# Optimization experiments

Hardware: AMD Instinct MI355X
Metric: run time of the kernel (lower is better)

The kernel has to match this reference:

```python
import jax, jax.numpy as jnp
import numpy as np

B, N, F, H = 64, 1024, 128, 256  # graphs, nodes per graph, nfeat, nhid


def setup_inputs() -> dict:
    key = jax.random.key(0)
    ks = jax.random.split(key, 8)
    s_in = 1.0 / np.sqrt(F)
    s_h = 1.0 / np.sqrt(H)
    return {
        "embs": jax.random.normal(ks[0], (B, N, F), jnp.float32),
        "adjmat": jax.random.uniform(ks[1], (B, N, N), jnp.float32) / N,  # row-scaled dense adjacency
        "W0": jax.random.normal(ks[2], (F, H), jnp.float32) * s_in,
        "b0": jnp.zeros((H,), jnp.float32),
        "W1": jax.random.normal(ks[3], (H, H), jnp.float32) * s_h,
        "b1": jnp.zeros((H,), jnp.float32),
        "W2": jax.random.normal(ks[4], (H, H), jnp.float32) * s_h,
        "b2": jnp.zeros((H,), jnp.float32),
        "Wl": jax.random.normal(ks[5], (H, F), jnp.float32) * s_h,
        "bl": jnp.zeros((F,), jnp.float32),
    }


def reference(embs, adjmat, W0, b0, W1, b1, W2, b2, Wl, bl):
    # Batched form of the per-graph loop: every adj is N x N, so the
    # x[:adj.shape[0]] slice is identity and all graphs fuse into one GEMM.
    hid = embs  # [B, N, F]
    for W, b in ((W0, b0), (W1, b1), (W2, b2)):
        # GraphConvolution: adj @ (x @ W) + b, then relu
        hid = jax.nn.relu(jnp.einsum('bnm,bmh->bnh', adjmat, hid @ W) + b)
    out = hid @ Wl + bl          # [B, N, F] linear_hid
    return out[:, 0, :]          # hid[0] per graph -> [B, F]
```

## Files before the change

kernel.cpp:

```cpp
#include <hip/hip_runtime.h>
#include <stdint.h>

typedef __bf16 bf16;
typedef __bf16 bf16x8 __attribute__((ext_vector_type(8)));
typedef float f32x4 __attribute__((ext_vector_type(4)));

enum { EPI_STORE = 0, EPI_BIAS_RELU = 1, EPI_VRED = 2 };

template<bool A_F32, bool B_F32, int EPI>
__global__ __launch_bounds__(256, 2)
void gemm_bt(const void* __restrict__ Ap, const void* __restrict__ Btp,
             const float* __restrict__ bias, bf16* __restrict__ C,
             float* __restrict__ vpart, const float* __restrict__ adjp,
             int K, int ldA, int ldBt, int ldC,
             long sA, long sBt, long sC)
{
  constexpr int BM = 128, BN = 256, BK = 32;
  __shared__ __align__(16) bf16 As[BM * BK];
  __shared__ __align__(16) bf16 Bs[BN * BK];
  __shared__ float a0s[BM];
  __shared__ float vsum[BN];

  const int tid  = threadIdx.x;
  const int lane = tid & 63;
  const int wid  = tid >> 6;
  const int wm   = wid >> 1;
  const int wn   = wid & 1;
  const int l15  = lane & 15;
  const int quad = lane >> 4;

  const int nb = blockIdx.x, mb = blockIdx.y, g = blockIdx.z;

  const long aoff = (long)g * sA + (long)mb * BM * ldA;
  const long boff = (long)g * sBt + (long)nb * BN * ldBt;

  if constexpr (EPI == EPI_VRED) {
    if (tid < BM) a0s[tid] = adjp[(long)g * sA + mb * BM + tid];
    vsum[tid] = 0.f;
  }

  f32x4 acc[4][8] = {};

  const int nsteps = K / BK;
  const int r  = tid >> 2;
  const int kc = (tid & 3) * 8;

  for (int ks = 0; ks < nsteps; ++ks) {
    const int k0 = ks * BK;
    __syncthreads();
    if constexpr (A_F32) {
      const float* Ag = (const float*)Ap + aoff + k0;
      #pragma unroll
      for (int p = 0; p < BM / 64; ++p) {
        const float4* s = (const float4*)(Ag + (long)(p * 64 + r) * ldA + kc);
        float4 v0 = s[0], v1 = s[1];
        bf16x8 w;
        w[0]=(bf16)v0.x; w[1]=(bf16)v0.y; w[2]=(bf16)v0.z; w[3]=(bf16)v0.w;
        w[4]=(bf16)v1.x; w[5]=(bf16)v1.y; w[6]=(bf16)v1.z; w[7]=(bf16)v1.w;
        *(bf16x8*)&As[p * 2048 + tid * 8] = w;
      }
    } else {
      const bf16* Ag = (const bf16*)Ap + aoff + k0;
      #pragma unroll
      for (int p = 0; p < BM / 64; ++p)
        *(bf16x8*)&As[p * 2048 + tid * 8] =
            *(const bf16x8*)(Ag + (long)(p * 64 + r) * ldA + kc);
    }
    if constexpr (B_F32) {
      const float* Bg = (const float*)Btp + boff + k0;
      #pragma unroll
      for (int p = 0; p < BN / 64; ++p) {
        const float4* s = (const float4*)(Bg + (long)(p * 64 + r) * ldBt + kc);
        float4 v0 = s[0], v1 = s[1];
        bf16x8 w;
        w[0]=(bf16)v0.x; w[1]=(bf16)v0.y; w[2]=(bf16)v0.z; w[3]=(bf16)v0.w;
        w[4]=(bf16)v1.x; w[5]=(bf16)v1.y; w[6]=(bf16)v1.z; w[7]=(bf16)v1.w;
        *(bf16x8*)&Bs[p * 2048 + tid * 8] = w;
      }
    } else {
      const bf16* Bg = (const bf16*)Btp + boff + k0;
      #pragma unroll
      for (int p = 0; p < BN / 64; ++p)
        *(bf16x8*)&Bs[p * 2048 + tid * 8] =
            *(const bf16x8*)(Bg + (long)(p * 64 + r) * ldBt + kc);
    }
    __syncthreads();

    bf16x8 af[4], bfr[8];
    #pragma unroll
    for (int i = 0; i < 4; ++i)
      af[i] = *(const bf16x8*)&As[(wm * 64 + i * 16 + l15) * BK + quad * 8];
    #pragma unroll
    for (int j = 0; j < 8; ++j)
      bfr[j] = *(const bf16x8*)&Bs[(wn * 128 + j * 16 + l15) * BK + quad * 8];
    #pragma unroll
    for (int i = 0; i < 4; ++i)
      #pragma unroll
      for (int j = 0; j < 8; ++j)
        acc[i][j] = __builtin_amdgcn_mfma_f32_16x16x32_bf16(af[i], bfr[j], acc[i][j], 0, 0, 0);
  }

  if constexpr (EPI == EPI_STORE || EPI == EPI_BIAS_RELU) {
    bf16* Cg = C + (long)g * sC;
    #pragma unroll
    for (int i = 0; i < 4; ++i) {
      const int row0 = mb * BM + wm * 64 + i * 16 + quad * 4;
      #pragma unroll
      for (int j = 0; j < 8; ++j) {
        const int col = nb * BN + wn * 128 + j * 16 + l15;
        float bv = 0.f;
        if constexpr (EPI == EPI_BIAS_RELU) bv = bias[col];
        #pragma unroll
        for (int rr = 0; rr < 4; ++rr) {
          float v = acc[i][j][rr];
          if constexpr (EPI == EPI_BIAS_RELU) v = fmaxf(v + bv, 0.f);
          Cg[(long)(row0 + rr) * ldC + col] = (bf16)v;
        }
      }
    }
  } else {
    __syncthreads();
    #pragma unroll
    for (int j = 0; j < 8; ++j) {
      const int col = wn * 128 + j * 16 + l15;
      const float bv = bias[col];
      float p = 0.f;
      #pragma unroll
      for (int i = 0; i < 4; ++i) {
        const int lr = wm * 64 + i * 16 + quad * 4;
        #pragma unroll
        for (int rr = 0; rr < 4; ++rr)
          p += fmaxf(acc[i][j][rr] + bv, 0.f) * a0s[lr + rr];
      }
      atomicAdd(&vsum[col], p);
    }
    __syncthreads();
    vpart[((long)g * 8 + mb) * 256 + tid] = vsum[tid];
  }
}

__global__ void prep_w(const float* __restrict__ W0, const float* __restrict__ W1,
                       bf16* __restrict__ W0t, bf16* __restrict__ W1t)
{
  const int idx = blockIdx.x * 256 + threadIdx.x;
  if (idx < 256 * 128) {
    const int h = idx >> 7, k = idx & 127;
    W0t[idx] = (bf16)W0[k * 256 + h];
  }
  const int h = idx >> 8, k = idx & 255;
  W1t[idx] = (bf16)W1[k * 256 + h];
}

__global__ void finish_k(const float* __restrict__ vpart, const float* __restrict__ W2,
                         const float* __restrict__ b2, const float* __restrict__ Wl,
                         const float* __restrict__ bl, float* __restrict__ out)
{
  const int b = blockIdx.x, t = threadIdx.x;
  __shared__ float v[256], h3[256];
  float s = 0.f;
  #pragma unroll
  for (int mb = 0; mb < 8; ++mb) s += vpart[((long)b * 8 + mb) * 256 + t];
  v[t] = s;
  __syncthreads();
  float z = b2[t];
  for (int k = 0; k < 256; ++k) z += v[k] * W2[k * 256 + t];
  h3[t] = fmaxf(z, 0.f);
  __syncthreads();
  if (t < 128) {
    float o = bl[t];
    for (int h = 0; h < 256; ++h) o += h3[h] * Wl[h * 128 + t];
    out[(long)b * 128 + t] = o;
  }
}

extern "C" void kernel_launch(void* const* d_in, const int* in_sizes, int n_in,
                              void* d_out, int out_size, void* d_ws, size_t ws_size,
                              hipStream_t stream) {
  const float* embs = (const float*)d_in[0];
  const float* adj  = (const float*)d_in[1];
  const float* W0   = (const float*)d_in[2];
  const float* b0   = (const float*)d_in[3];
  const float* W1   = (const float*)d_in[4];
  const float* b1   = (const float*)d_in[5];
  const float* W2   = (const float*)d_in[6];
  const float* b2   = (const float*)d_in[7];
  const float* Wl   = (const float*)d_in[8];
  const float* bl   = (const float*)d_in[9];
  float* out = (float*)d_out;

  char* ws = (char*)d_ws;
  bf16*  Zt    = (bf16*)(ws);
  bf16*  Hb    = (bf16*)(ws + 33554432);
  bf16*  W0t   = (bf16*)(ws + 67108864);
  bf16*  W1t   = (bf16*)(ws + 67174400);
  float* vpart = (float*)(ws + 67305472);

  prep_w<<<256, 256, 0, stream>>>(W0, W1, W0t, W1t);

  gemm_bt<false, true, EPI_STORE><<<dim3(4, 2, 64), 256, 0, stream>>>(
      W0t, embs, nullptr, Zt, nullptr, nullptr,
      128, 128, 128, 1024, 0L, 131072L, 262144L);

  gemm_bt<true, false, EPI_BIAS_RELU><<<dim3(1, 8, 64), 256, 0, stream>>>(
      adj, Zt, b0, Hb, nullptr, nullptr,
      1024, 1024, 1024, 256, 1048576L, 262144L, 262144L);

  gemm_bt<false, false, EPI_STORE><<<dim3(4, 2, 64), 256, 0, stream>>>(
      W1t, Hb, nullptr, Zt, nullptr, nullptr,
      256, 256, 256, 1024, 0L, 262144L, 262144L);

  gemm_bt<true, false, EPI_VRED><<<dim3(1, 8, 64), 256, 0, stream>>>(
      adj, Zt, b1, nullptr, vpart, adj,
      1024, 1024, 1024, 256, 1048576L, 262144L, 0L);

  finish_k<<<64, 256, 0, stream>>>(vpart, W2, b2, Wl, bl, out);
}
```

Baseline: 569.6 us.

## Pre-convert adjacency to bf16 and stream tiles via direct global-to-LDS loads

Adds a conversion kernel that turns adj and embs into bf16 buffers once, so both adjacency GEMMs read half the bytes instead of converting fp32 in registers twice. The GEMM loads now use global_load_lds so tiles go straight into shared memory without passing through registers. BM is halved to 64 with occupancy hint 3, doubling the grid and the partial-sum count in finish_k. The cost is an extra full pass over the 256MB fp32 adjacency plus a 128MB bf16 write, and an extra kernel launch.

```diff
diff --git a/kernel.cpp b/kernel.cpp
--- a/kernel.cpp
+++ b/kernel.cpp
@@ -7,15 +7,20 @@
 
 enum { EPI_STORE = 0, EPI_BIAS_RELU = 1, EPI_VRED = 2 };
 
-template<bool A_F32, bool B_F32, int EPI>
-__global__ __launch_bounds__(256, 2)
-void gemm_bt(const void* __restrict__ Ap, const void* __restrict__ Btp,
+__device__ __forceinline__ void load_lds16(const bf16* g, bf16* l) {
+  __builtin_amdgcn_global_load_lds((const __attribute__((address_space(1))) void*)g,
+                                   (__attribute__((address_space(3))) void*)l, 16, 0, 0);
+}
+
+template<int EPI>
+__global__ __launch_bounds__(256, 3)
+void gemm_bt(const bf16* __restrict__ Ap, const bf16* __restrict__ Btp,
              const float* __restrict__ bias, bf16* __restrict__ C,
-             float* __restrict__ vpart, const float* __restrict__ adjp,
+             float* __restrict__ vpart, const bf16* __restrict__ a0p,
              int K, int ldA, int ldBt, int ldC,
              long sA, long sBt, long sC)
 {
-  constexpr int BM = 128, BN = 256, BK = 32;
+  constexpr int BM = 64, BN = 256, BK = 32;
   __shared__ __align__(16) bf16 As[BM * BK];
   __shared__ __align__(16) bf16 Bs[BN * BK];
   __shared__ float a0s[BM];
@@ -24,77 +29,41 @@
   const int tid  = threadIdx.x;
   const int lane = tid & 63;
   const int wid  = tid >> 6;
-  const int wm   = wid >> 1;
-  const int wn   = wid & 1;
+  const int wm   = wid & 1;
+  const int wn   = wid >> 1;
   const int l15  = lane & 15;
   const int quad = lane >> 4;
 
   const int nb = blockIdx.x, mb = blockIdx.y, g = blockIdx.z;
 
-  const long aoff = (long)g * sA + (long)mb * BM * ldA;
-  const long boff = (long)g * sBt + (long)nb * BN * ldBt;
+  const bf16* Ag = Ap + (long)g * sA + (long)(mb * BM + (tid >> 2)) * ldA + (tid & 3) * 8;
+  const bf16* Bg = Btp + (long)g * sBt + (long)(nb * BN + (tid >> 2)) * ldBt + (tid & 3) * 8;
+  const long bstep = (long)64 * ldBt;
 
   if constexpr (EPI == EPI_VRED) {
-    if (tid < BM) a0s[tid] = adjp[(long)g * sA + mb * BM + tid];
+    if (tid < BM) a0s[tid] = (float)a0p[(long)g * sA + mb * BM + tid];
     vsum[tid] = 0.f;
   }
 
-  f32x4 acc[4][8] = {};
-
-  const int nsteps = K / BK;
-  const int r  = tid >> 2;
-  const int kc = (tid & 3) * 8;
-
-  for (int ks = 0; ks < nsteps; ++ks) {
-    const int k0 = ks * BK;
-    __syncthreads();
-    if constexpr (A_F32) {
-      const float* Ag = (const float*)Ap + aoff + k0;
-      #pragma unroll
-      for (int p = 0; p < BM / 64; ++p) {
-        const float4* s = (const float4*)(Ag + (long)(p * 64 + r) * ldA + kc);
-        float4 v0 = s[0], v1 = s[1];
-        bf16x8 w;
-        w[0]=(bf16)v0.x; w[1]=(bf16)v0.y; w[2]=(bf16)v0.z; w[3]=(bf16)v0.w;
-        w[4]=(bf16)v1.x; w[5]=(bf16)v1.y; w[6]=(bf16)v1.z; w[7]=(bf16)v1.w;
-        *(bf16x8*)&As[p * 2048 + tid * 8] = w;
-      }
-    } else {
-      const bf16* Ag = (const bf16*)Ap + aoff + k0;
-      #pragma unroll
-      for (int p = 0; p < BM / 64; ++p)
-        *(bf16x8*)&As[p * 2048 + tid * 8] =
-            *(const bf16x8*)(Ag + (long)(p * 64 + r) * ldA + kc);
-    }
-    if constexpr (B_F32) {
-      const float* Bg = (const float*)Btp + boff + k0;
-      #pragma unroll
-      for (int p = 0; p < BN / 64; ++p) {
-        const float4* s = (const float4*)(Bg + (long)(p * 64 + r) * ldBt + kc);
-        float4 v0 = s[0], v1 = s[1];
-        bf16x8 w;
-        w[0]=(bf16)v0.x; w[1]=(bf16)v0.y; w[2]=(bf16)v0.z; w[3]=(bf16)v0.w;
-        w[4]=(bf16)v1.x; w[5]=(bf16)v1.y; w[6]=(bf16)v1.z; w[7]=(bf16)v1.w;
-        *(bf16x8*)&Bs[p * 2048 + tid * 8] = w;
-      }
-    } else {
-      const bf16* Bg = (const bf16*)Btp + boff + k0;
-      #pragma unroll
-      for (int p = 0; p < BN / 64; ++p)
-        *(bf16x8*)&Bs[p * 2048 + tid * 8] =
-            *(const bf16x8*)(Bg + (long)(p * 64 + r) * ldBt + kc);
-    }
-    __syncthreads();
-
-    bf16x8 af[4], bfr[8];
-    #pragma unroll
-    for (int i = 0; i < 4; ++i)
-      af[i] = *(const bf16x8*)&As[(wm * 64 + i * 16 + l15) * BK + quad * 8];
+  f32x4 acc[2][8] = {};
+
+  for (int ks = 0; ks < K; ks += BK) {
+    __syncthreads();
+    load_lds16(Ag + ks, As + tid * 8);
+    #pragma unroll
+    for (int p = 0; p < 4; ++p)
+      load_lds16(Bg + p * bstep + ks, Bs + p * 2048 + tid * 8);
+    __syncthreads();
+
+    bf16x8 af[2], bfr[8];
+    #pragma unroll
+    for (int i = 0; i < 2; ++i)
+      af[i] = *(const bf16x8*)&As[(wm * 32 + i * 16 + l15) * BK + quad * 8];
     #pragma unroll
     for (int j = 0; j < 8; ++j)
       bfr[j] = *(const bf16x8*)&Bs[(wn * 128 + j * 16 + l15) * BK + quad * 8];
     #pragma unroll
-    for (int i = 0; i < 4; ++i)
+    for (int i = 0; i < 2; ++i)
       #pragma unroll
       for (int j = 0; j < 8; ++j)
         acc[i][j] = __builtin_amdgcn_mfma_f32_16x16x32_bf16(af[i], bfr[j], acc[i][j], 0, 0, 0);
@@ -103,8 +72,8 @@
   if constexpr (EPI == EPI_STORE || EPI == EPI_BIAS_RELU) {
     bf16* Cg = C + (long)g * sC;
     #pragma unroll
-    for (int i = 0; i < 4; ++i) {
-      const int row0 = mb * BM + wm * 64 + i * 16 + quad * 4;
+    for (int i = 0; i < 2; ++i) {
+      const int row0 = mb * BM + wm * 32 + i * 16 + quad * 4;
       #pragma unroll
       for (int j = 0; j < 8; ++j) {
         const int col = nb * BN + wn * 128 + j * 16 + l15;
@@ -126,8 +95,8 @@
       const float bv = bias[col];
       float p = 0.f;
       #pragma unroll
-      for (int i = 0; i < 4; ++i) {
-        const int lr = wm * 64 + i * 16 + quad * 4;
+      for (int i = 0; i < 2; ++i) {
+        const int lr = wm * 32 + i * 16 + quad * 4;
         #pragma unroll
         for (int rr = 0; rr < 4; ++rr)
           p += fmaxf(acc[i][j][rr] + bv, 0.f) * a0s[lr + rr];
@@ -135,8 +104,23 @@
       atomicAdd(&vsum[col], p);
     }
     __syncthreads();
-    vpart[((long)g * 8 + mb) * 256 + tid] = vsum[tid];
-  }
+    vpart[((long)g * 16 + mb) * 256 + tid] = vsum[tid];
+  }
+}
+
+__global__ void cvt_prep(const float* __restrict__ adj, const float* __restrict__ embs,
+                         bf16* __restrict__ adjb, bf16* __restrict__ embsb)
+{
+  const long c = (long)blockIdx.x * 256 + threadIdx.x;
+  const float* src; bf16* dst; long off;
+  if (c < 8388608) { src = adj;  dst = adjb;  off = c * 8; }
+  else             { src = embs; dst = embsb; off = (c - 8388608) * 8; }
+  float4 v0 = *(const float4*)(src + off);
+  float4 v1 = *(const float4*)(src + off + 4);
+  bf16x8 w;
+  w[0]=(bf16)v0.x; w[1]=(bf16)v0.y; w[2]=(bf16)v0.z; w[3]=(bf16)v0.w;
+  w[4]=(bf16)v1.x; w[5]=(bf16)v1.y; w[6]=(bf16)v1.z; w[7]=(bf16)v1.w;
+  *(bf16x8*)(dst + off) = w;
 }
 
 __global__ void prep_w(const float* __restrict__ W0, const float* __restrict__ W1,
@@ -159,7 +143,7 @@
   __shared__ float v[256], h3[256];
   float s = 0.f;
   #pragma unroll
-  for (int mb = 0; mb < 8; ++mb) s += vpart[((long)b * 8 + mb) * 256 + t];
+  for (int mb = 0; mb < 16; ++mb) s += vpart[((long)b * 16 + mb) * 256 + t];
   v[t] = s;
   __syncthreads();
   float z = b2[t];
@@ -189,28 +173,31 @@
   float* out = (float*)d_out;
 
   char* ws = (char*)d_ws;
-  bf16*  Zt    = (bf16*)(ws);
-  bf16*  Hb    = (bf16*)(ws + 33554432);
-  bf16*  W0t   = (bf16*)(ws + 67108864);
-  bf16*  W1t   = (bf16*)(ws + 67174400);
-  float* vpart = (float*)(ws + 67305472);
-
+  bf16*  adjb  = (bf16*)(ws);
+  bf16*  embsb = (bf16*)(ws + 134217728);
+  bf16*  Zt    = (bf16*)(ws + 150994944);
+  bf16*  Hb    = (bf16*)(ws + 184549376);
+  bf16*  W0t   = (bf16*)(ws + 218103808);
+  bf16*  W1t   = (bf16*)(ws + 218169344);
+  float* vpart = (float*)(ws + 218300416);
+
+  cvt_prep<<<36864, 256, 0, stream>>>(adj, embs, adjb, embsb);
   prep_w<<<256, 256, 0, stream>>>(W0, W1, W0t, W1t);
 
-  gemm_bt<false, true, EPI_STORE><<<dim3(4, 2, 64), 256, 0, stream>>>(
-      W0t, embs, nullptr, Zt, nullptr, nullptr,
+  gemm_bt<EPI_STORE><<<dim3(4, 4, 64), 256, 0, stream>>>(
+      W0t, embsb, nullptr, Zt, nullptr, nullptr,
       128, 128, 128, 1024, 0L, 131072L, 262144L);
 
-  gemm_bt<true, false, EPI_BIAS_RELU><<<dim3(1, 8, 64), 256, 0, stream>>>(
-      adj, Zt, b0, Hb, nullptr, nullptr,
+  gemm_bt<EPI_BIAS_RELU><<<dim3(1, 16, 64), 256, 0, stream>>>(
+      adjb, Zt, b0, Hb, nullptr, nullptr,
       1024, 1024, 1024, 256, 1048576L, 262144L, 262144L);
 
-  gemm_bt<false, false, EPI_STORE><<<dim3(4, 2, 64), 256, 0, stream>>>(
+  gemm_bt<EPI_STORE><<<dim3(4, 4, 64), 256, 0, stream>>>(
       W1t, Hb, nullptr, Zt, nullptr, nullptr,
       256, 256, 256, 1024, 0L, 262144L, 262144L);
 
-  gemm_bt<true, false, EPI_VRED><<<dim3(1, 8, 64), 256, 0, stream>>>(
-      adj, Zt, b1, nullptr, vpart, adj,
+  gemm_bt<EPI_VRED><<<dim3(1, 16, 64), 256, 0, stream>>>(
+      adjb, Zt, b1, nullptr, vpart, adjb,
       1024, 1024, 1024, 256, 1048576L, 262144L, 0L);
 
   finish_k<<<64, 256, 0, stream>>>(vpart, W2, b2, Wl, bl, out);
```

After: 619.7 us. 8.8% more time.
